# Optimization experiments

Measured on AMD Instinct MI355X. Metric: run time of the kernel, lower is better.

Reference implementation:

```python
import jax, jax.numpy as jnp
import numpy as np

N = 100000
E = 3200000
F_IN = 512
NUM_CLASSES = 8
H1, C1 = 4, 8   # conv1: 4 heads, 8 channels each (concat -> 32)
H2, C2 = 1, NUM_CLASSES  # conv2: 1 head, mean (concat=False)
NEG_SLOPE = 0.2


def gat_conv(x, W, att_src, att_dst, bias, src, dst, num_nodes, concat):
    """PyG-style GATConv (eval mode, self-loops already in src/dst)."""
    H, C = att_src.shape
    xp = (x @ W).reshape(-1, H, C)              # [N, H, C]
    a_s = (xp * att_src[None]).sum(-1)           # [N, H]
    a_d = (xp * att_dst[None]).sum(-1)           # [N, H]
    e = jax.nn.leaky_relu(a_s[src] + a_d[dst], NEG_SLOPE)  # [E, H]
    # segment softmax over destination nodes (stable)
    e_max = jax.ops.segment_max(e, dst, num_segments=num_nodes)
    e = jnp.exp(e - e_max[dst])
    denom = jax.ops.segment_sum(e, dst, num_segments=num_nodes)
    alpha = e / denom[dst]                        # [E, H]
    msg = xp[src] * alpha[..., None]              # [E, H, C]
    out = jax.ops.segment_sum(msg, dst, num_segments=num_nodes)  # [N, H, C]
    if concat:
        out = out.reshape(num_nodes, H * C)
    else:
        out = out.mean(axis=1)
    return out + bias


def setup_inputs() -> dict:
    key = jax.random.key(0)
    ks = jax.random.split(key, 9)
    s = 0.1
    return {
        "x": jax.random.normal(ks[0], (N, F_IN), dtype=jnp.float32),
        "edge_index": jax.random.randint(ks[1], (2, E), 0, N, dtype=jnp.int32),
        "W1": jax.random.normal(ks[2], (F_IN, H1 * C1), dtype=jnp.float32) * s,
        "att_src1": jax.random.normal(ks[3], (H1, C1), dtype=jnp.float32) * s,
        "att_dst1": jax.random.normal(ks[4], (H1, C1), dtype=jnp.float32) * s,
        "b1": jnp.zeros((H1 * C1,), dtype=jnp.float32),
        "W2": jax.random.normal(ks[5], (H1 * C1, H2 * C2), dtype=jnp.float32) * s,
        "att_src2": jax.random.normal(ks[6], (H2, C2), dtype=jnp.float32) * s,
        "att_dst2": jax.random.normal(ks[7], (H2, C2), dtype=jnp.float32) * s,
        "b2": jnp.zeros((C2,), dtype=jnp.float32),
    }


def reference(x, edge_index, W1, att_src1, att_dst1, b1, W2, att_src2, att_dst2, b2):
    # PyG GATConv default add_self_loops=True
    loop = jnp.arange(N, dtype=edge_index.dtype)
    src = jnp.concatenate([edge_index[0], loop])
    dst = jnp.concatenate([edge_index[1], loop])
    # dropout is identity in eval mode
    h = jax.nn.elu(gat_conv(x, W1, att_src1, att_dst1, b1, src, dst, N, True))
    out = gat_conv(h, W2, att_src2, att_dst2, b2, src, dst, N, False)
    return out
```

## Files before the change

kernel.cpp:

```cpp
#include <hip/hip_runtime.h>

typedef unsigned short u16;
typedef unsigned int   u32;

#define NN  100000
#define EE  3200000
#define ETOT 3300000
#define FIN 512
#define NBUK 1024
#define NPB  98
#define CAP  4096
#define TILE_A 16384
#define NBLK_A ((ETOT + TILE_A - 1) / TILE_A)
#define NBLK_G ((NN + 63) / 64)

typedef __attribute__((ext_vector_type(8))) short bfx8;
typedef __attribute__((ext_vector_type(4))) float f32x4;

__device__ __forceinline__ float bf2f(u16 u){ return __uint_as_float(((u32)u) << 16); }
__device__ __forceinline__ float lo16f(u32 v){ return __uint_as_float(v << 16); }
__device__ __forceinline__ float hi16f(u32 v){ return __uint_as_float(v & 0xffff0000u); }
__device__ __forceinline__ u16 f2bf(float f){
  u32 u = __float_as_uint(f);
  u += 0x7fffu + ((u >> 16) & 1u);
  return (u16)(u >> 16);
}
__device__ __forceinline__ u32 pack2(float a, float b){
  return ((u32)f2bf(b) << 16) | (u32)f2bf(a);
}

__device__ __forceinline__ void binA_body(int blk, const int* __restrict__ ei,
                                          u32* __restrict__ gcnt,
                                          u32* __restrict__ buk,
                                          u32* hcnt){
  int t = threadIdx.x;
  for (int q = t; q < NBUK; q += 256) hcnt[q] = 0;
  __syncthreads();
  int e0 = blk * TILE_A;
  #pragma unroll 4
  for (int i = 0; i < TILE_A/256; i++){
    int e = e0 + i*256 + t;
    if (e < ETOT){
      int d = (e < EE) ? ei[EE + e] : (e - EE);
      atomicAdd(&hcnt[(u32)d / NPB], 1u);
    }
  }
  __syncthreads();
  for (int q = t; q < NBUK; q += 256){
    u32 c = hcnt[q];
    if (c) hcnt[q] = ((u32)q << 12) + atomicAdd(&gcnt[q], c);
  }
  __syncthreads();
  #pragma unroll 4
  for (int i = 0; i < TILE_A/256; i++){
    int e = e0 + i*256 + t;
    if (e < ETOT){
      int s, d;
      if (e < EE){ s = ei[e]; d = ei[EE + e]; } else { s = e - EE; d = s; }
      u32 b = (u32)d / NPB;
      u32 r = atomicAdd(&hcnt[b], 1u);
      buk[r] = ((u32)(d - (int)b*NPB) << 17) | (u32)s;
    }
  }
}

__device__ __forceinline__ void gemm_body(int gb,
    const float* __restrict__ x, const u16* __restrict__ WTb,
    const float* __restrict__ attS, const float* __restrict__ attD,
    u16* __restrict__ xp1, float* __restrict__ as1, float* __restrict__ ad1){
  int tid = threadIdx.x;
  int nb  = gb * 64;

  int lane = tid & 63, wid = tid >> 6;
  int m = lane & 15, quad = lane >> 4;
  int rowbase = wid * 16;
  int row = nb + rowbase + m; if (row >= NN) row = NN - 1;
  const float* xrow = x + (size_t)row * FIN + quad * 8;
  const u16* b0g = WTb + m * FIN + quad * 8;
  const u16* b1g = b0g + 16 * FIN;

  f32x4 acc0 = {0.f, 0.f, 0.f, 0.f};
  f32x4 acc1 = {0.f, 0.f, 0.f, 0.f};

  union Ubf { bfx8 v; u32 u[4]; };

  #pragma unroll
  for (int kc = 0; kc < 4; kc++){
    #pragma unroll
    for (int ks = 0; ks < 4; ks++){
      const float4* g = (const float4*)(xrow + kc*128 + ks*32);
      float4 f0 = g[0], f1 = g[1];
      Ubf ua;
      ua.u[0] = pack2(f0.x, f0.y); ua.u[1] = pack2(f0.z, f0.w);
      ua.u[2] = pack2(f1.x, f1.y); ua.u[3] = pack2(f1.z, f1.w);
      bfx8 b0 = *(const bfx8*)(b0g + kc*128 + ks*32);
      bfx8 b1 = *(const bfx8*)(b1g + kc*128 + ks*32);
      acc0 = __builtin_amdgcn_mfma_f32_16x16x32_bf16(ua.v, b0, acc0, 0, 0, 0);
      acc1 = __builtin_amdgcn_mfma_f32_16x16x32_bf16(ua.v, b1, acc1, 0, 0, 0);
    }
  }

  #pragma unroll
  for (int t = 0; t < 2; t++){
    f32x4 acc = t ? acc1 : acc0;
    int colg = t*16 + m;
    float aS = attS[colg], aD = attD[colg];
    #pragma unroll
    for (int r = 0; r < 4; r++){
      int node = nb + rowbase + quad*4 + r;
      float v = acc[r];
      if (node < NN) xp1[(size_t)node*32 + colg] = f2bf(v);
      float ps = v * aS, pd = v * aD;
      ps += __shfl_xor(ps, 1); ps += __shfl_xor(ps, 2); ps += __shfl_xor(ps, 4);
      pd += __shfl_xor(pd, 1); pd += __shfl_xor(pd, 2); pd += __shfl_xor(pd, 4);
      if ((m & 7) == 0 && node < NN){
        as1[node*4 + (colg >> 3)] = ps;
        ad1[node*4 + (colg >> 3)] = pd;
      }
    }
  }
}


__global__ void __launch_bounds__(256) k_fat(const int* __restrict__ ei,
    u32* __restrict__ gcnt, u32* __restrict__ buk,
    const float* __restrict__ x, const u16* __restrict__ WTb,
    const float* __restrict__ attS, const float* __restrict__ attD,
    u16* __restrict__ xp1, float* __restrict__ as1, float* __restrict__ ad1){
  __shared__ u32 sm[NBUK];
  if (blockIdx.x < NBLK_A)
    binA_body(blockIdx.x, ei, gcnt, buk, sm);
  else
    gemm_body(blockIdx.x - NBLK_A, x, WTb, attS, attD, xp1, as1, ad1);
}

__global__ void __launch_bounds__(256) k_binA(const int* __restrict__ ei,
                                              u32* __restrict__ gcnt,
                                              u32* __restrict__ buk){
  __shared__ u32 sm2[NBUK];
  binA_body(blockIdx.x, ei, gcnt, buk, sm2);
}

__global__ void __launch_bounds__(256) k_gemm1(
    const float* __restrict__ x, const u16* __restrict__ WTb,
    const float* __restrict__ attS, const float* __restrict__ attD,
    u16* __restrict__ xp1, float* __restrict__ as1, float* __restrict__ ad1){
  gemm_body(blockIdx.x, x, WTb, attS, attD, xp1, as1, ad1);
}

__global__ void __launch_bounds__(256) k_scatterB(const u32* __restrict__ gcnt,
                                                  const u32* __restrict__ buk,
                                                  int2* __restrict__ range,
                                                  int* __restrict__ srcs){
  __shared__ u32 dcnt[NPB + 1];
  __shared__ u32 cur[NPB];
  __shared__ u32 red[256];
  int b = blockIdx.x, t = threadIdx.x;
  u32 acc = 0;
  for (int i = t; i < b; i += 256) acc += gcnt[i];
  red[t] = acc;
  if (t < NPB + 1) dcnt[t] = 0;
  __syncthreads();
  for (int o = 128; o > 0; o >>= 1){
    if (t < o) red[t] += red[t + o];
    __syncthreads();
  }
  u32 gb = red[0];
  u32 lo = (u32)b << 12;
  u32 hi = lo + gcnt[b];
  for (u32 j = lo + t; j < hi; j += 256)
    atomicAdd(&dcnt[(buk[j] >> 17) + 1], 1u);
  __syncthreads();
  for (int o = 1; o < 128; o <<= 1){
    u32 x = 0;
    if (t < NPB + 1 && t >= o) x = dcnt[t - o];
    __syncthreads();
    if (t < NPB + 1 && t >= o) dcnt[t] += x;
    __syncthreads();
  }
  if (t < NPB){
    u32 beg = gb + dcnt[t];
    cur[t] = beg;
    int node = b * NPB + t;
    if (node < NN){
      range[node] = make_int2((int)beg, (int)(gb + dcnt[t + 1]));
    }
  }
  __syncthreads();
  for (u32 j = lo + t; j < hi; j += 256){
    u32 p = buk[j];
    u32 pos = atomicAdd(&cur[p >> 17], 1u);
    srcs[pos] = (int)(p & 0x1FFFFu);
  }
}

__global__ void k_prep_w(const float* __restrict__ W1, u16* __restrict__ WTb,
                         u32* __restrict__ gcnt){
  int i = blockIdx.x*blockDim.x + threadIdx.x;
  if (i < NBUK) gcnt[i] = 0;
  if (i >= FIN*32) return;
  int k = i >> 5, c = i & 31;
  WTb[c*FIN + k] = f2bf(W1[i]);
}

__global__ void __launch_bounds__(256) k_agg1(
    const int2* __restrict__ range, const int* __restrict__ srcs,
    const u32* __restrict__ xp1u, const float* __restrict__ as1,
    const float* __restrict__ ad1, const float* __restrict__ b1,
    u32* __restrict__ hfeatu){
  int wid = (blockIdx.x * 256 + threadIdx.x) >> 6;
  if (wid >= NN) return;
  int lane = threadIdx.x & 63;
  int e = lane >> 4;
  int l = lane & 15;
  int h = l >> 2;
  int2 rr = range[wid];
  int beg = rr.x, end = rr.y;
  float ad = ad1[wid*4 + h];
  float num0 = 0.f, num1 = 0.f, den = 0.f;
  int j = beg + e;
  for (; j + 12 < end; j += 16){
    int s0 = srcs[j], s1 = srcs[j + 4], s2 = srcs[j + 8], s3 = srcs[j + 12];
    u32 v0 = xp1u[(size_t)s0*16 + l];
    u32 v1 = xp1u[(size_t)s1*16 + l];
    u32 v2 = xp1u[(size_t)s2*16 + l];
    u32 v3 = xp1u[(size_t)s3*16 + l];
    float z0 = as1[s0*4 + h] + ad;
    float z1 = as1[s1*4 + h] + ad;
    float z2 = as1[s2*4 + h] + ad;
    float z3 = as1[s3*4 + h] + ad;
    z0 = (z0 >= 0.f) ? z0 : 0.2f * z0;
    z1 = (z1 >= 0.f) ? z1 : 0.2f * z1;
    z2 = (z2 >= 0.f) ? z2 : 0.2f * z2;
    z3 = (z3 >= 0.f) ? z3 : 0.2f * z3;
    float w0 = __expf(z0), w1 = __expf(z1), w2 = __expf(z2), w3 = __expf(z3);
    num0 = fmaf(w0, lo16f(v0), num0); num1 = fmaf(w0, hi16f(v0), num1); den += w0;
    num0 = fmaf(w1, lo16f(v1), num0); num1 = fmaf(w1, hi16f(v1), num1); den += w1;
    num0 = fmaf(w2, lo16f(v2), num0); num1 = fmaf(w2, hi16f(v2), num1); den += w2;
    num0 = fmaf(w3, lo16f(v3), num0); num1 = fmaf(w3, hi16f(v3), num1); den += w3;
  }
  if (j + 4 < end){
    int s0 = srcs[j], s1 = srcs[j + 4];
    u32 v0 = xp1u[(size_t)s0*16 + l];
    u32 v1 = xp1u[(size_t)s1*16 + l];
    float z0 = as1[s0*4 + h] + ad;
    float z1 = as1[s1*4 + h] + ad;
    z0 = (z0 >= 0.f) ? z0 : 0.2f * z0;
    z1 = (z1 >= 0.f) ? z1 : 0.2f * z1;
    float w0 = __expf(z0), w1 = __expf(z1);
    num0 = fmaf(w0, lo16f(v0), num0); num1 = fmaf(w0, hi16f(v0), num1); den += w0;
    num0 = fmaf(w1, lo16f(v1), num0); num1 = fmaf(w1, hi16f(v1), num1); den += w1;
    j += 8;
  }
  for (; j < end; j += 4){
    int s0 = srcs[j];
    u32 v0 = xp1u[(size_t)s0*16 + l];
    float z0 = as1[s0*4 + h] + ad;
    z0 = (z0 >= 0.f) ? z0 : 0.2f * z0;
    float w0 = __expf(z0);
    num0 = fmaf(w0, lo16f(v0), num0); num1 = fmaf(w0, hi16f(v0), num1); den += w0;
  }
  num0 += __shfl_xor(num0, 16); num0 += __shfl_xor(num0, 32);
  num1 += __shfl_xor(num1, 16); num1 += __shfl_xor(num1, 32);
  den  += __shfl_xor(den, 16);  den  += __shfl_xor(den, 32);
  if (e == 0){
    float o0 = num0 / den + b1[2*l];
    float o1 = num1 / den + b1[2*l + 1];
    o0 = (o0 > 0.f) ? o0 : (__expf(o0) - 1.f);
    o1 = (o1 > 0.f) ? o1 : (__expf(o1) - 1.f);
    hfeatu[(size_t)wid*16 + l] = pack2(o0, o1);
  }
}

__global__ void k_feat2(const u16* __restrict__ hfeat, const float* __restrict__ W2,
                        const float* __restrict__ attS, const float* __restrict__ attD,
                        float* __restrict__ xp2, float* __restrict__ as2,
                        float* __restrict__ ad2){
  int n = blockIdx.x*blockDim.x + threadIdx.x;
  if (n >= NN) return;
  const u16* hr = hfeat + (size_t)n*32;
  float h[32];
  #pragma unroll
  for (int k = 0; k < 32; k++) h[k] = bf2f(hr[k]);
  float o[8];
  #pragma unroll
  for (int j = 0; j < 8; j++) o[j] = 0.f;
  #pragma unroll
  for (int k = 0; k < 32; k++){
    #pragma unroll
    for (int j = 0; j < 8; j++) o[j] = fmaf(h[k], W2[k*8 + j], o[j]);
  }
  float s = 0.f, d = 0.f;
  #pragma unroll
  for (int j = 0; j < 8; j++){
    xp2[(size_t)n*8 + j] = o[j];
    s = fmaf(o[j], attS[j], s);
    d = fmaf(o[j], attD[j], d);
  }
  as2[n] = s; ad2[n] = d;
}

__global__ void __launch_bounds__(256) k_agg2(
    const int2* __restrict__ range, const int* __restrict__ srcs,
    const float* __restrict__ xp2, const float* __restrict__ as2,
    const float* __restrict__ ad2, const float* __restrict__ b2,
    float* __restrict__ out){
  int wid = (blockIdx.x * 256 + threadIdx.x) >> 6;
  if (wid >= NN) return;
  int lane = threadIdx.x & 63;
  int p = lane >> 3, c = lane & 7;
  int2 rr = range[wid];
  int beg = rr.x, end = rr.y;
  float ad = ad2[wid];
  float num = 0.f, den = 0.f;
  int j = beg + p;
  for (; j + 24 < end; j += 32){
    int s0 = srcs[j], s1 = srcs[j + 8], s2 = srcs[j + 16], s3 = srcs[j + 24];
    float v0 = xp2[(size_t)s0*8 + c];
    float v1 = xp2[(size_t)s1*8 + c];
    float v2 = xp2[(size_t)s2*8 + c];
    float v3 = xp2[(size_t)s3*8 + c];
    float z0 = as2[s0] + ad;
    float z1 = as2[s1] + ad;
    float z2 = as2[s2] + ad;
    float z3 = as2[s3] + ad;
    z0 = (z0 >= 0.f) ? z0 : 0.2f * z0;
    z1 = (z1 >= 0.f) ? z1 : 0.2f * z1;
    z2 = (z2 >= 0.f) ? z2 : 0.2f * z2;
    z3 = (z3 >= 0.f) ? z3 : 0.2f * z3;
    float w0 = __expf(z0), w1 = __expf(z1), w2 = __expf(z2), w3 = __expf(z3);
    num = fmaf(w0, v0, num); den += w0;
    num = fmaf(w1, v1, num); den += w1;
    num = fmaf(w2, v2, num); den += w2;
    num = fmaf(w3, v3, num); den += w3;
  }
  if (j + 8 < end){
    int s0 = srcs[j], s1 = srcs[j + 8];
    float v0 = xp2[(size_t)s0*8 + c];
    float v1 = xp2[(size_t)s1*8 + c];
    float z0 = as2[s0] + ad;
    float z1 = as2[s1] + ad;
    z0 = (z0 >= 0.f) ? z0 : 0.2f * z0;
    z1 = (z1 >= 0.f) ? z1 : 0.2f * z1;
    float w0 = __expf(z0), w1 = __expf(z1);
    num = fmaf(w0, v0, num); den += w0;
    num = fmaf(w1, v1, num); den += w1;
    j += 16;
  }
  for (; j < end; j += 8){
    int s0 = srcs[j];
    float v0 = xp2[(size_t)s0*8 + c];
    float z0 = as2[s0] + ad;
    z0 = (z0 >= 0.f) ? z0 : 0.2f * z0;
    float w0 = __expf(z0);
    num = fmaf(w0, v0, num); den += w0;
  }
  num += __shfl_xor(num, 8);  den += __shfl_xor(den, 8);
  num += __shfl_xor(num, 16); den += __shfl_xor(den, 16);
  num += __shfl_xor(num, 32); den += __shfl_xor(den, 32);
  if (p == 0){
    out[(size_t)wid*8 + c] = num / den + b2[c];
  }
}

extern "C" void kernel_launch(void* const* d_in, const int* in_sizes, int n_in,
                              void* d_out, int out_size, void* d_ws, size_t ws_size,
                              hipStream_t stream){
  (void)in_sizes; (void)n_in; (void)out_size;
  const float* x   = (const float*)d_in[0];
  const int*   ei  = (const int*)d_in[1];
  const float* W1  = (const float*)d_in[2];
  const float* aS1 = (const float*)d_in[3];
  const float* aD1 = (const float*)d_in[4];
  const float* b1  = (const float*)d_in[5];
  const float* W2  = (const float*)d_in[6];
  const float* aS2 = (const float*)d_in[7];
  const float* aD2 = (const float*)d_in[8];
  const float* b2  = (const float*)d_in[9];
  float* out = (float*)d_out;

  char* w = (char*)d_ws;
  auto alloc = [&](size_t bytes) -> char* {
    char* p = w; w += (bytes + 15) & ~(size_t)15; return p;
  };

  int2*  range  = (int2*)alloc((size_t)NN*8);
  int*   srcs   = (int*)alloc((size_t)ETOT*4);
  u16*   xp1    = (u16*)alloc((size_t)NN*64);
  float* as1    = (float*)alloc((size_t)NN*16);
  float* ad1    = (float*)alloc((size_t)NN*16);
  u16*   hfeat  = (u16*)alloc((size_t)NN*64);
  float* xp2    = (float*)alloc((size_t)NN*32);
  float* as2    = (float*)alloc((size_t)NN*4);
  float* ad2    = (float*)alloc((size_t)NN*4);
  u16*   WTb    = (u16*)alloc(32*512*2);
  u32*   gcnt   = (u32*)alloc(NBUK*4);
  size_t base_need = (size_t)(w - (char*)d_ws);
  size_t buk_bytes = (size_t)NBUK * CAP * 4;
  bool overlap = (ws_size >= base_need + buk_bytes);

  u32* buk;
  if (overlap){
    buk = (u32*)alloc(buk_bytes);
  } else {
    buk = (u32*)xp1;
  }

  k_prep_w  <<<64, 256, 0, stream>>>(W1, WTb, gcnt);
  if (overlap){
    k_fat   <<<NBLK_A + NBLK_G, 256, 0, stream>>>(ei, gcnt, buk, x, WTb, aS1, aD1,
                                                  xp1, as1, ad1);
    k_scatterB<<<NBUK, 256, 0, stream>>>(gcnt, buk, range, srcs);
  } else {
    k_binA  <<<NBLK_A, 256, 0, stream>>>(ei, gcnt, buk);
    k_scatterB<<<NBUK, 256, 0, stream>>>(gcnt, buk, range, srcs);
    k_gemm1 <<<NBLK_G, 256, 0, stream>>>(x, WTb, aS1, aD1, xp1, as1, ad1);
  }
  k_agg1    <<<NN/4, 256, 0, stream>>>(range, srcs, (const u32*)xp1, as1, ad1, b1, (u32*)hfeat);
  k_feat2   <<<(NN+255)/256, 256, 0, stream>>>(hfeat, W2, aS2, aD2, xp2, as2, ad2);
  k_agg2    <<<NN/4, 256, 0, stream>>>(range, srcs, xp2, as2, ad2, b2, out);
}
```

Baseline: 510.4 us.

## Split GEMM work across binning and scatter kernels, batch loads, use hardware bf16 pack

The layer-1 GEMM blocks are now split between two fused kernels. The first 600 tiles run alongside the edge-binning pass and the rest alongside the scatter pass, so both index-building phases get independent MFMA work to overlap with. Inside the GEMM, all x and W loads for a k-chunk are issued before conversion and MFMA to expose more memory parallelism. The software round-to-nearest bf16 packing is replaced with the v_cvt_pk_bf16_f32 instruction. The trade-offs are a fixed split ratio that may not match the phase durations, higher register pressure from the batched loads, and possibly different rounding behaviour from the hardware conversion.

```diff
diff --git a/kernel.cpp b/kernel.cpp
--- a/kernel.cpp
+++ b/kernel.cpp
@@ -13,6 +13,8 @@
 #define TILE_A 16384
 #define NBLK_A ((ETOT + TILE_A - 1) / TILE_A)
 #define NBLK_G ((NN + 63) / 64)
+#define G1 600
+#define G2 (NBLK_G - G1)
 
 typedef __attribute__((ext_vector_type(8))) short bfx8;
 typedef __attribute__((ext_vector_type(4))) float f32x4;
@@ -27,6 +29,11 @@
 }
 __device__ __forceinline__ u32 pack2(float a, float b){
   return ((u32)f2bf(b) << 16) | (u32)f2bf(a);
+}
+__device__ __forceinline__ u32 cvtpk(float a, float b){
+  u32 r;
+  asm("v_cvt_pk_bf16_f32 %0, %1, %2" : "=v"(r) : "v"(a), "v"(b));
+  return r;
 }
 
 __device__ __forceinline__ void binA_body(int blk, const int* __restrict__ ei,
@@ -86,17 +93,28 @@
 
   #pragma unroll
   for (int kc = 0; kc < 4; kc++){
+    float4 fx[8];
     #pragma unroll
     for (int ks = 0; ks < 4; ks++){
       const float4* g = (const float4*)(xrow + kc*128 + ks*32);
-      float4 f0 = g[0], f1 = g[1];
+      fx[2*ks]   = g[0];
+      fx[2*ks+1] = g[1];
+    }
+    bfx8 b0v[4], b1v[4];
+    #pragma unroll
+    for (int ks = 0; ks < 4; ks++){
+      b0v[ks] = *(const bfx8*)(b0g + kc*128 + ks*32);
+      b1v[ks] = *(const bfx8*)(b1g + kc*128 + ks*32);
+    }
+    #pragma unroll
+    for (int ks = 0; ks < 4; ks++){
       Ubf ua;
-      ua.u[0] = pack2(f0.x, f0.y); ua.u[1] = pack2(f0.z, f0.w);
-      ua.u[2] = pack2(f1.x, f1.y); ua.u[3] = pack2(f1.z, f1.w);
-      bfx8 b0 = *(const bfx8*)(b0g + kc*128 + ks*32);
-      bfx8 b1 = *(const bfx8*)(b1g + kc*128 + ks*32);
-      acc0 = __builtin_amdgcn_mfma_f32_16x16x32_bf16(ua.v, b0, acc0, 0, 0, 0);
-      acc1 = __builtin_amdgcn_mfma_f32_16x16x32_bf16(ua.v, b1, acc1, 0, 0, 0);
+      ua.u[0] = cvtpk(fx[2*ks].x,   fx[2*ks].y);
+      ua.u[1] = cvtpk(fx[2*ks].z,   fx[2*ks].w);
+      ua.u[2] = cvtpk(fx[2*ks+1].x, fx[2*ks+1].y);
+      ua.u[3] = cvtpk(fx[2*ks+1].z, fx[2*ks+1].w);
+      acc0 = __builtin_amdgcn_mfma_f32_16x16x32_bf16(ua.v, b0v[ks], acc0, 0, 0, 0);
+      acc1 = __builtin_amdgcn_mfma_f32_16x16x32_bf16(ua.v, b1v[ks], acc1, 0, 0, 0);
     }
   }
 
@@ -121,8 +139,54 @@
   }
 }
 
-
-__global__ void __launch_bounds__(256) k_fat(const int* __restrict__ ei,
+__device__ __forceinline__ void scatterB_body(int b, const u32* __restrict__ gcnt,
+                                              const u32* __restrict__ buk,
+                                              int2* __restrict__ range,
+                                              int* __restrict__ srcs){
+  __shared__ u32 dcnt[NPB + 1];
+  __shared__ u32 cur[NPB];
+  __shared__ u32 red[256];
+  int t = threadIdx.x;
+  u32 acc = 0;
+  for (int i = t; i < b; i += 256) acc += gcnt[i];
+  red[t] = acc;
+  if (t < NPB + 1) dcnt[t] = 0;
+  __syncthreads();
+  for (int o = 128; o > 0; o >>= 1){
+    if (t < o) red[t] += red[t + o];
+    __syncthreads();
+  }
+  u32 gb = red[0];
+  u32 lo = (u32)b << 12;
+  u32 hi = lo + gcnt[b];
+  for (u32 j = lo + t; j < hi; j += 256)
+    atomicAdd(&dcnt[(buk[j] >> 17) + 1], 1u);
+  __syncthreads();
+  for (int o = 1; o < 128; o <<= 1){
+    u32 x = 0;
+    if (t < NPB + 1 && t >= o) x = dcnt[t - o];
+    __syncthreads();
+    if (t < NPB + 1 && t >= o) dcnt[t] += x;
+    __syncthreads();
+  }
+  if (t < NPB){
+    u32 beg = gb + dcnt[t];
+    cur[t] = beg;
+    int node = b * NPB + t;
+    if (node < NN){
+      range[node] = make_int2((int)beg, (int)(gb + dcnt[t + 1]));
+    }
+  }
+  __syncthreads();
+  for (u32 j = lo + t; j < hi; j += 256){
+    u32 p = buk[j];
+    u32 pos = atomicAdd(&cur[p >> 17], 1u);
+    srcs[pos] = (int)(p & 0x1FFFFu);
+  }
+}
+
+
+__global__ void __launch_bounds__(256) k_fat1(const int* __restrict__ ei,
     u32* __restrict__ gcnt, u32* __restrict__ buk,
     const float* __restrict__ x, const u16* __restrict__ WTb,
     const float* __restrict__ attS, const float* __restrict__ attD,
@@ -134,6 +198,18 @@
     gemm_body(blockIdx.x - NBLK_A, x, WTb, attS, attD, xp1, as1, ad1);
 }
 
+__global__ void __launch_bounds__(256) k_fat2(
+    const u32* __restrict__ gcnt, const u32* __restrict__ buk,
+    int2* __restrict__ range, int* __restrict__ srcs,
+    const float* __restrict__ x, const u16* __restrict__ WTb,
+    const float* __restrict__ attS, const float* __restrict__ attD,
+    u16* __restrict__ xp1, float* __restrict__ as1, float* __restrict__ ad1){
+  if (blockIdx.x < NBUK)
+    scatterB_body(blockIdx.x, gcnt, buk, range, srcs);
+  else
+    gemm_body(G1 + (int)blockIdx.x - NBUK, x, WTb, attS, attD, xp1, as1, ad1);
+}
+
 __global__ void __launch_bounds__(256) k_binA(const int* __restrict__ ei,
                                               u32* __restrict__ gcnt,
                                               u32* __restrict__ buk){
@@ -152,46 +228,7 @@
                                                   const u32* __restrict__ buk,
                                                   int2* __restrict__ range,
                                                   int* __restrict__ srcs){
-  __shared__ u32 dcnt[NPB + 1];
-  __shared__ u32 cur[NPB];
-  __shared__ u32 red[256];
-  int b = blockIdx.x, t = threadIdx.x;
-  u32 acc = 0;
-  for (int i = t; i < b; i += 256) acc += gcnt[i];
-  red[t] = acc;
-  if (t < NPB + 1) dcnt[t] = 0;
-  __syncthreads();
-  for (int o = 128; o > 0; o >>= 1){
-    if (t < o) red[t] += red[t + o];
-    __syncthreads();
-  }
-  u32 gb = red[0];
-  u32 lo = (u32)b << 12;
-  u32 hi = lo + gcnt[b];
-  for (u32 j = lo + t; j < hi; j += 256)
-    atomicAdd(&dcnt[(buk[j] >> 17) + 1], 1u);
-  __syncthreads();
-  for (int o = 1; o < 128; o <<= 1){
-    u32 x = 0;
-    if (t < NPB + 1 && t >= o) x = dcnt[t - o];
-    __syncthreads();
-    if (t < NPB + 1 && t >= o) dcnt[t] += x;
-    __syncthreads();
-  }
-  if (t < NPB){
-    u32 beg = gb + dcnt[t];
-    cur[t] = beg;
-    int node = b * NPB + t;
-    if (node < NN){
-      range[node] = make_int2((int)beg, (int)(gb + dcnt[t + 1]));
-    }
-  }
-  __syncthreads();
-  for (u32 j = lo + t; j < hi; j += 256){
-    u32 p = buk[j];
-    u32 pos = atomicAdd(&cur[p >> 17], 1u);
-    srcs[pos] = (int)(p & 0x1FFFFu);
-  }
+  scatterB_body(blockIdx.x, gcnt, buk, range, srcs);
 }
 
 __global__ void k_prep_w(const float* __restrict__ W1, u16* __restrict__ WTb,
@@ -408,9 +445,10 @@
 
   k_prep_w  <<<64, 256, 0, stream>>>(W1, WTb, gcnt);
   if (overlap){
-    k_fat   <<<NBLK_A + NBLK_G, 256, 0, stream>>>(ei, gcnt, buk, x, WTb, aS1, aD1,
-                                                  xp1, as1, ad1);
-    k_scatterB<<<NBUK, 256, 0, stream>>>(gcnt, buk, range, srcs);
+    k_fat1  <<<NBLK_A + G1, 256, 0, stream>>>(ei, gcnt, buk, x, WTb, aS1, aD1,
+                                              xp1, as1, ad1);
+    k_fat2  <<<NBUK + G2, 256, 0, stream>>>(gcnt, buk, range, srcs, x, WTb,
+                                            aS1, aD1, xp1, as1, ad1);
   } else {
     k_binA  <<<NBLK_A, 256, 0, stream>>>(ei, gcnt, buk);
     k_scatterB<<<NBUK, 256, 0, stream>>>(gcnt, buk, range, srcs);
```

Measured after the change: 524.1 us. +2.7%, slower.
